# Kernel optimization log

Hardware: AMD Instinct MI355X
Metric: run time of the kernel (lower is better)

The kernel has to match this reference:

```python
import jax, jax.numpy as jnp
import numpy as np

B, S, D, H = 4, 2048, 1024, 16
DK = D // H

def setup_inputs() -> dict:
    key = jax.random.key(0)
    ks = jax.random.split(key, 9)
    sc = 1.0 / np.sqrt(D)
    return {
        "X": jax.random.normal(ks[0], (B, S, D), jnp.float32),
        "Wq": jax.random.normal(ks[1], (D, D), jnp.float32) * sc,
        "bq": jax.random.normal(ks[2], (D,), jnp.float32) * 0.01,
        "Wk": jax.random.normal(ks[3], (D, D), jnp.float32) * sc,
        "bk": jax.random.normal(ks[4], (D,), jnp.float32) * 0.01,
        "Wv": jax.random.normal(ks[5], (D, D), jnp.float32) * sc,
        "bv": jax.random.normal(ks[6], (D,), jnp.float32) * 0.01,
        "Wo": jax.random.normal(ks[7], (D, D), jnp.float32) * sc,
        "bo": jax.random.normal(ks[8], (D,), jnp.float32) * 0.01,
    }

def _split_heads(x):
    b, s, d = x.shape
    return x.reshape(b, s, H, DK).transpose(0, 2, 1, 3)  # [B,H,S,DK]

def reference(X, Wq, bq, Wk, bk, Wv, bv, Wo, bo):
    Q = _split_heads(X @ Wq + bq)
    K = _split_heads(X @ Wk + bk)
    V = _split_heads(X @ Wv + bv)
    scores = jnp.einsum('bhqd,bhkd->bhqk', Q, K) / np.sqrt(DK)  # [B,H,S,S]
    probs = jax.nn.softmax(scores, axis=-1)
    Z = jnp.einsum('bhqk,bhkd->bhqd', probs, V)  # [B,H,S,DK]
    Z = Z.transpose(0, 2, 1, 3).reshape(B, S, D)  # combine heads
    return Z @ Wo + bo
```

## Files before the change

kernel.cpp:

```cpp
#include <hip/hip_runtime.h>

#define Bq 4
#define Sq 2048
#define Dq 1024
#define Hq 16
#define Mq (Bq*Sq)

typedef __attribute__((ext_vector_type(2))) _Float16 f16x2;
typedef __attribute__((ext_vector_type(4))) _Float16 f16x4;
typedef __attribute__((ext_vector_type(8))) _Float16 f16x8;
typedef __attribute__((ext_vector_type(4))) float f32x4;

__device__ __forceinline__ f16x2 cvt_pk_f16(float a, float b) {
  return __builtin_bit_cast(f16x2, __builtin_amdgcn_cvt_pkrtz(a, b));
}

__device__ __forceinline__ float fast_exp2(float x) {
#if __has_builtin(__builtin_amdgcn_exp2f)
  return __builtin_amdgcn_exp2f(x);
#else
  float r;
  asm volatile("v_exp_f32 %0, %1\n\ts_nop 0" : "=v"(r) : "v"(x));
  return r;
#endif
}

__device__ __forceinline__ void gload16(const _Float16* g, _Float16* l) {
  __builtin_amdgcn_global_load_lds(
      (const __attribute__((address_space(1))) unsigned int*)g,
      (__attribute__((address_space(3))) unsigned int*)l, 16, 0, 0);
}

#define VMCNT(n) asm volatile("s_waitcnt vmcnt(" #n ")" ::: "memory")
#define BARRIER() do { __builtin_amdgcn_s_barrier(); __builtin_amdgcn_sched_barrier(0); } while (0)
#define MFMA32(a, b, c) __builtin_amdgcn_mfma_f32_16x16x32_f16(a, b, c, 0, 0, 0)

__global__ void cvt_f32_f16(const float* __restrict__ in, _Float16* __restrict__ out, int n4) {
  int i = blockIdx.x * blockDim.x + threadIdx.x;
  int stride = gridDim.x * blockDim.x;
  for (; i < n4; i += stride) {
    float4 v = ((const float4*)in)[i];
    f16x4 h = { (_Float16)v.x, (_Float16)v.y, (_Float16)v.z, (_Float16)v.w };
    ((f16x4*)out)[i] = h;
  }
}

__global__ __launch_bounds__(256)
void wt_cvt_T(const float* __restrict__ W, _Float16* __restrict__ WT) {
  __shared__ _Float16 Tw[64][68];
  const int t = threadIdx.x;
  const int k0 = blockIdx.x * 64, n0 = blockIdx.y * 64;
  #pragma unroll
  for (int i = 0; i < 4; i++) {
    int row = (t >> 4) + 16 * i;
    float4 v = *(const float4*)(W + (size_t)(k0 + row) * Dq + n0 + (t & 15) * 4);
    f16x4 h = { (_Float16)v.x, (_Float16)v.y, (_Float16)v.z, (_Float16)v.w };
    *(f16x4*)&Tw[row][(t & 15) * 4] = h;
  }
  __syncthreads();
  const int n = t & 63, ks = t >> 6;
  f16x8 v0, v1;
  #pragma unroll
  for (int j = 0; j < 8; j++) { v0[j] = Tw[ks * 16 + j][n]; v1[j] = Tw[ks * 16 + 8 + j][n]; }
  _Float16* dst = WT + (size_t)(n0 + n) * Dq + k0 + ks * 16;
  *(f16x8*)dst = v0;
  *(f16x8*)(dst + 8) = v1;
}

__global__ __launch_bounds__(256, 3)
void qkv_gemm(const _Float16* __restrict__ A, const _Float16* __restrict__ WTall,
              const float* __restrict__ bq, const float* __restrict__ bk,
              const float* __restrict__ bv, _Float16* __restrict__ Qh,
              _Float16* __restrict__ Kh, _Float16* __restrict__ Vth, float qscale) {
  __shared__ alignas(16) char smem[33280];
  _Float16* As = (_Float16*)smem;
  _Float16* Bs = (_Float16*)(smem + 16384);
  const int tid = threadIdx.x, wid = tid >> 6, lane = tid & 63;
  const int wr = wid >> 1, wc = wid & 1;
  const int lq = lane & 15, g = lane >> 4;
  int bid = (int)blockIdx.x;
  bid = (bid & 7) * 192 + (bid >> 3);
  const int bx = bid % 24, by = bid / 24;
  const int row0 = by * 128, col0 = bx * 128;

  const int srow = lane >> 3;
  const int schunk = (lane & 7) ^ srow;
  const _Float16* Ag = A     + (size_t)(row0 + 32 * wid + srow) * Dq + schunk * 8;
  const _Float16* Bg = WTall + (size_t)(col0 + 32 * wid + srow) * Dq + schunk * 8;
  _Float16* AsW = As + (32 * wid) * 64;
  _Float16* BsW = Bs + (32 * wid) * 64;

  f32x4 acc[4][4];
  #pragma unroll
  for (int m = 0; m < 4; m++)
    #pragma unroll
    for (int n = 0; n < 4; n++) acc[m][n] = (f32x4){0.f, 0.f, 0.f, 0.f};

  for (int k0 = 0; k0 < Dq; k0 += 64) {
    __syncthreads();
    #pragma unroll
    for (int i = 0; i < 4; i++) {
      gload16(Ag + k0 + (size_t)(8 * i) * Dq, AsW + (8 * i) * 64);
      gload16(Bg + k0 + (size_t)(8 * i) * Dq, BsW + (8 * i) * 64);
    }
    __syncthreads();
    #pragma unroll
    for (int s = 0; s < 2; s++) {
      f16x8 a[4], b[4];
      #pragma unroll
      for (int m = 0; m < 4; m++) {
        int row = wr * 64 + m * 16 + lq;
        a[m] = *(const f16x8*)&As[row * 64 + (((4 * s + g) ^ (lq & 7)) * 8)];
      }
      #pragma unroll
      for (int n = 0; n < 4; n++) {
        int row = wc * 64 + n * 16 + lq;
        b[n] = *(const f16x8*)&Bs[row * 64 + (((4 * s + g) ^ (lq & 7)) * 8)];
      }
      #pragma unroll
      for (int m = 0; m < 4; m++)
        #pragma unroll
        for (int n = 0; n < 4; n++)
          acc[m][n] = MFMA32(a[m], b[n], acc[m][n]);
    }
  }

  const int rid = col0 >> 10, lcol0 = col0 & 1023;
  const float* bp = rid == 0 ? bq : (rid == 1 ? bk : bv);
  const float scl = rid == 0 ? qscale : 1.0f;

  if (rid < 2) {
    _Float16* Cc = rid == 0 ? Qh : Kh;
    #pragma unroll
    for (int m = 0; m < 4; m++)
      #pragma unroll
      for (int n = 0; n < 4; n++) {
        int col = lcol0 + wc * 64 + n * 16 + lq;
        float bvv = bp[col];
        #pragma unroll
        for (int r = 0; r < 4; r++) {
          int row = row0 + wr * 64 + m * 16 + 4 * g + r;
          Cc[(size_t)row * Dq + col] = (_Float16)((acc[m][n][r] + bvv) * scl);
        }
      }
  } else {
    _Float16* Ts = (_Float16*)smem;
    __syncthreads();
    #pragma unroll
    for (int m = 0; m < 4; m++)
      #pragma unroll
      for (int n = 0; n < 4; n++) {
        int c = wc * 64 + n * 16 + lq;
        float bvv = bp[lcol0 + c];
        #pragma unroll
        for (int r = 0; r < 4; r++) {
          int s = wr * 64 + m * 16 + 4 * g + r;
          Ts[s * 130 + c] = (_Float16)(acc[m][n][r] + bvv);
        }
      }
    __syncthreads();
    const int b = row0 >> 11, stile = (row0 & 2047) >> 7;
    #pragma unroll
    for (int i = 0; i < 8; i++) {
      int idx = i * 256 + tid;
      int hh = idx >> 10, c = idx & 1023;
      int kk = c >> 8, nd = (c >> 6) & 3, gg = (c >> 4) & 3, lqq = c & 15;
      int d = nd * 16 + lqq;
      f16x8 v;
      #pragma unroll
      for (int j = 0; j < 8; j++) {
        int sl = 32 * kk + 16 * (j >> 2) + 4 * gg + (j & 3);
        v[j] = Ts[sl * 130 + hh * 64 + d];
      }
      int hHead = (lcol0 >> 6) + hh;
      size_t off = (((size_t)(b * Hq + hHead) * 16 + stile) * 1024 + c) * 8;
      *(f16x8*)(Vth + off) = v;
    }
  }
}

__global__ __launch_bounds__(256, 3)
void out_gemm(const _Float16* __restrict__ A, const _Float16* __restrict__ WT,
              const float* __restrict__ bias, float* __restrict__ Cf) {
  __shared__ alignas(16) char smem[32768];
  _Float16* As = (_Float16*)smem;
  _Float16* Bs = (_Float16*)(smem + 16384);
  const int tid = threadIdx.x, wid = tid >> 6, lane = tid & 63;
  const int wr = wid >> 1, wc = wid & 1;
  const int lq = lane & 15, g = lane >> 4;
  int bid = (int)blockIdx.x;
  bid = (bid & 7) * 64 + (bid >> 3);
  const int bx = bid & 7, by = bid >> 3;
  const int row0 = by * 128, col0 = bx * 128;

  const int srow = lane >> 3;
  const int schunk = (lane & 7) ^ srow;
  const _Float16* Ag = A  + (size_t)(row0 + 32 * wid + srow) * Dq + schunk * 8;
  const _Float16* Bg = WT + (size_t)(col0 + 32 * wid + srow) * Dq + schunk * 8;
  _Float16* AsW = As + (32 * wid) * 64;
  _Float16* BsW = Bs + (32 * wid) * 64;

  f32x4 acc[4][4];
  #pragma unroll
  for (int m = 0; m < 4; m++)
    #pragma unroll
    for (int n = 0; n < 4; n++) acc[m][n] = (f32x4){0.f, 0.f, 0.f, 0.f};

  for (int k0 = 0; k0 < Dq; k0 += 64) {
    __syncthreads();
    #pragma unroll
    for (int i = 0; i < 4; i++) {
      gload16(Ag + k0 + (size_t)(8 * i) * Dq, AsW + (8 * i) * 64);
      gload16(Bg + k0 + (size_t)(8 * i) * Dq, BsW + (8 * i) * 64);
    }
    __syncthreads();
    #pragma unroll
    for (int s = 0; s < 2; s++) {
      f16x8 a[4], b[4];
      #pragma unroll
      for (int m = 0; m < 4; m++) {
        int row = wr * 64 + m * 16 + lq;
        a[m] = *(const f16x8*)&As[row * 64 + (((4 * s + g) ^ (lq & 7)) * 8)];
      }
      #pragma unroll
      for (int n = 0; n < 4; n++) {
        int row = wc * 64 + n * 16 + lq;
        b[n] = *(const f16x8*)&Bs[row * 64 + (((4 * s + g) ^ (lq & 7)) * 8)];
      }
      #pragma unroll
      for (int m = 0; m < 4; m++)
        #pragma unroll
        for (int n = 0; n < 4; n++)
          acc[m][n] = MFMA32(a[m], b[n], acc[m][n]);
    }
  }

  #pragma unroll
  for (int m = 0; m < 4; m++)
    #pragma unroll
    for (int n = 0; n < 4; n++) {
      int col = col0 + wc * 64 + n * 16 + lq;
      float bvv = bias[col];
      #pragma unroll
      for (int r = 0; r < 4; r++) {
        int row = row0 + wr * 64 + m * 16 + 4 * g + r;
        Cf[(size_t)row * Dq + col] = acc[m][n][r] + bvv;
      }
    }
}

__global__ __launch_bounds__(256, 4)
void attn_kernel(const _Float16* __restrict__ Q, const _Float16* __restrict__ K,
                 const _Float16* __restrict__ Vt, _Float16* __restrict__ Z) {
  __shared__ alignas(16) char smem[32768];
  _Float16* const sm = (_Float16*)smem;
  const int tid = threadIdx.x, wid = tid >> 6, lane = tid & 63;
  const int lq = lane & 15, g = lane >> 4;
  const int id = (int)blockIdx.x;
  const int qb = (id >> 3) & 15;
  const int hb = (id & 7) + 8 * (id >> 7);
  const int h = hb & 15, b = hb >> 4;
  const int q0 = qb * 128;
  const int bh = b * Hq + h;

  const _Float16* Qr0 = Q + (size_t)(b * Sq + q0 + wid * 32 + lq) * Dq + h * 64;
  const _Float16* Qr1 = Qr0 + (size_t)16 * Dq;
  const f16x8 Qf00 = *(const f16x8*)(Qr0 + 8 * g);
  const f16x8 Qf01 = *(const f16x8*)(Qr0 + 32 + 8 * g);
  const f16x8 Qf10 = *(const f16x8*)(Qr1 + 8 * g);
  const f16x8 Qf11 = *(const f16x8*)(Qr1 + 32 + 8 * g);
  VMCNT(0);

  const int krow = tid >> 3;
  const int kch = (tid & 7) ^ (krow & 7);
  const _Float16* Kg = K + (size_t)(b * Sq + krow) * Dq + h * 64 + kch * 8;
  const _Float16* Vg = Vt + (size_t)bh * 16 * 8192;

  const int e7 = lq & 7;
  const int cq0 = (g ^ e7) * 8, cq1 = ((4 + g) ^ e7) * 8;

  f32x4 zacc[2][4];
  #pragma unroll
  for (int gq = 0; gq < 2; gq++)
    #pragma unroll
    for (int nd = 0; nd < 4; nd++) zacc[gq][nd] = (f32x4){0.f, 0.f, 0.f, 0.f};
  f32x4 lsum0 = (f32x4){0.f, 0.f, 0.f, 0.f};
  f32x4 lsum1 = (f32x4){0.f, 0.f, 0.f, 0.f};
  const f32x4 fz = (f32x4){0.f, 0.f, 0.f, 0.f};
  f16x8 ones;
  #pragma unroll
  for (int j = 0; j < 8; j++) ones[j] = (_Float16)1.0f;

  auto stageK = [&](int t, int buf) {
    _Float16* Kd = sm + buf * 4096;
    const _Float16* ks = Kg + (size_t)t * 64 * Dq;
    gload16(ks, Kd + tid * 8);
    gload16(ks + (size_t)32 * Dq, Kd + 2048 + tid * 8);
  };
  auto stageV = [&](int t, int buf) {
    _Float16* Vd = sm + 8192 + buf * 4096;
    const _Float16* vs = Vg + (size_t)(t >> 1) * 8192 + (t & 1) * 4096 + tid * 8;
    gload16(vs, Vd + tid * 8);
    gload16(vs + 2048, Vd + 2048 + tid * 8);
  };

  stageK(0, 0);
  stageV(0, 0);

  for (int t = 0; t < 32; ++t) {
    const int buf = t & 1;
    const _Float16* Kb = sm + buf * 4096;
    const _Float16* Vb = sm + 8192 + buf * 4096;

    if (t) BARRIER();
    if (t < 31) { stageK(t + 1, buf ^ 1); stageV(t + 1, buf ^ 1); VMCNT(4); }
    else        { VMCNT(0); }
    BARRIER();

    f32x4 sacc[2][4];
    __builtin_amdgcn_s_setprio(1);
    #pragma unroll
    for (int rb = 0; rb < 4; ++rb) {
      const _Float16* rbp = Kb + (rb * 16 + lq) * 64;
      f16x8 a0 = *(const f16x8*)(rbp + cq0);
      f16x8 a1 = *(const f16x8*)(rbp + cq1);
      sacc[0][rb] = MFMA32(a0, Qf00, fz);
      sacc[0][rb] = MFMA32(a1, Qf01, sacc[0][rb]);
      sacc[1][rb] = MFMA32(a0, Qf10, fz);
      sacc[1][rb] = MFMA32(a1, Qf11, sacc[1][rb]);
    }
    __builtin_amdgcn_s_setprio(0);

    f16x8 pb[2][2];
    #pragma unroll
    for (int gq = 0; gq < 2; ++gq)
      #pragma unroll
      for (int kkL = 0; kkL < 2; ++kkL) {
        const f32x4 sa = sacc[gq][kkL * 2], sb = sacc[gq][kkL * 2 + 1];
        f16x2 c0 = cvt_pk_f16(fast_exp2(sa[0]), fast_exp2(sa[1]));
        f16x2 c1 = cvt_pk_f16(fast_exp2(sa[2]), fast_exp2(sa[3]));
        f16x2 c2 = cvt_pk_f16(fast_exp2(sb[0]), fast_exp2(sb[1]));
        f16x2 c3 = cvt_pk_f16(fast_exp2(sb[2]), fast_exp2(sb[3]));
        f16x8 p8;
        p8[0] = c0[0]; p8[1] = c0[1]; p8[2] = c1[0]; p8[3] = c1[1];
        p8[4] = c2[0]; p8[5] = c2[1]; p8[6] = c3[0]; p8[7] = c3[1];
        pb[gq][kkL] = p8;
      }

    __builtin_amdgcn_s_setprio(1);
    #pragma unroll
    for (int kkL = 0; kkL < 2; ++kkL) {
      lsum0 = MFMA32(ones, pb[0][kkL], lsum0);
      lsum1 = MFMA32(ones, pb[1][kkL], lsum1);
      #pragma unroll
      for (int nd = 0; nd < 4; ++nd) {
        f16x8 av = *(const f16x8*)(Vb + kkL * 2048 + nd * 512 + lane * 8);
        zacc[0][nd] = MFMA32(av, pb[0][kkL], zacc[0][nd]);
        zacc[1][nd] = MFMA32(av, pb[1][kkL], zacc[1][nd]);
      }
    }
    __builtin_amdgcn_s_setprio(0);
  }

  const float inv0 = 1.0f / lsum0[0];
  const float inv1 = 1.0f / lsum1[0];
  __syncthreads();
  _Float16* Zs = sm;
  #pragma unroll
  for (int gq = 0; gq < 2; gq++) {
    const float inv = gq == 0 ? inv0 : inv1;
    #pragma unroll
    for (int nd = 0; nd < 4; nd++) {
      f16x4 zv;
      #pragma unroll
      for (int r = 0; r < 4; r++) zv[r] = (_Float16)(zacc[gq][nd][r] * inv);
      *(f16x4*)&Zs[(wid * 32 + gq * 16 + lq) * 72 + nd * 16 + 4 * g] = zv;
    }
  }
  __syncthreads();
  const int row = tid >> 1, half = tid & 1;
  const _Float16* zr = &Zs[row * 72 + half * 32];
  f16x8 v0 = *(const f16x8*)zr;
  f16x8 v1 = *(const f16x8*)(zr + 8);
  f16x8 v2 = *(const f16x8*)(zr + 16);
  f16x8 v3 = *(const f16x8*)(zr + 24);
  _Float16* dst = Z + (size_t)(b * Sq + q0 + row) * Dq + h * 64 + half * 32;
  *(f16x8*)dst = v0;
  *(f16x8*)(dst + 8) = v1;
  *(f16x8*)(dst + 16) = v2;
  *(f16x8*)(dst + 24) = v3;
}

extern "C" void kernel_launch(void* const* d_in, const int* in_sizes, int n_in,
                              void* d_out, int out_size, void* d_ws, size_t ws_size,
                              hipStream_t stream) {
  const float* X  = (const float*)d_in[0];
  const float* Wq = (const float*)d_in[1];
  const float* bq = (const float*)d_in[2];
  const float* Wk = (const float*)d_in[3];
  const float* bk = (const float*)d_in[4];
  const float* Wv = (const float*)d_in[5];
  const float* bv = (const float*)d_in[6];
  const float* Wo = (const float*)d_in[7];
  const float* bo = (const float*)d_in[8];

  _Float16* Xh   = (_Float16*)d_ws;
  _Float16* WqT  = Xh   + (size_t)Mq * Dq;
  _Float16* WkT  = WqT  + (size_t)Dq * Dq;
  _Float16* WvT  = WkT  + (size_t)Dq * Dq;
  _Float16* WoT  = WvT  + (size_t)Dq * Dq;
  _Float16* Qh   = WoT  + (size_t)Dq * Dq;
  _Float16* Kh   = Qh   + (size_t)Mq * Dq;
  _Float16* Vth  = Kh   + (size_t)Mq * Dq;
  _Float16* Zh   = Vth  + (size_t)Mq * Dq;

  cvt_f32_f16<<<dim3(2048), dim3(256), 0, stream>>>(X, Xh, (int)((size_t)Mq * Dq / 4));
  dim3 wt(16, 16);
  wt_cvt_T<<<wt, dim3(256), 0, stream>>>(Wq, WqT);
  wt_cvt_T<<<wt, dim3(256), 0, stream>>>(Wk, WkT);
  wt_cvt_T<<<wt, dim3(256), 0, stream>>>(Wv, WvT);
  wt_cvt_T<<<wt, dim3(256), 0, stream>>>(Wo, WoT);

  const float qscale = 0.125f * 1.44269504088896f;
  qkv_gemm<<<dim3(1536), dim3(256), 0, stream>>>(Xh, WqT, bq, bk, bv, Qh, Kh, Vth, qscale);

  attn_kernel<<<dim3(1024), dim3(256), 0, stream>>>(Qh, Kh, Vth, Zh);

  out_gemm<<<dim3(512), dim3(256), 0, stream>>>(Zh, WoT, bo, (float*)d_out);
}
```

Measured before the change: 174.8 us.

## Merge weight conversions into one launch and deepen attention K/V prefetch

The four weight transpose-and-convert launches are merged into a single kernel that selects the weight matrix by block index. The attention loop now prefetches K/V two tiles ahead: it stages tiles 0 and 1 up front and refills a buffer right after its compute, with a barrier in between. The loop is also unrolled by two. The s_nop after the fallback v_exp_f32 asm is dropped. Together these aim to cut launch overhead and hide global load latency, at the cost of an extra barrier per iteration and possible exp hazard timing in the fallback path.

```diff
diff --git a/kernel.cpp b/kernel.cpp
--- a/kernel.cpp
+++ b/kernel.cpp
@@ -20,7 +20,7 @@
   return __builtin_amdgcn_exp2f(x);
 #else
   float r;
-  asm volatile("v_exp_f32 %0, %1\n\ts_nop 0" : "=v"(r) : "v"(x));
+  asm volatile("v_exp_f32 %0, %1" : "=v"(r) : "v"(x));
   return r;
 #endif
 }
@@ -46,10 +46,16 @@
 }
 
 __global__ __launch_bounds__(256)
-void wt_cvt_T(const float* __restrict__ W, _Float16* __restrict__ WT) {
+void wt_cvt_all(const float* __restrict__ W0, const float* __restrict__ W1,
+                const float* __restrict__ W2, const float* __restrict__ W3,
+                _Float16* __restrict__ WTbase) {
   __shared__ _Float16 Tw[64][68];
   const int t = threadIdx.x;
-  const int k0 = blockIdx.x * 64, n0 = blockIdx.y * 64;
+  const int bIdx = (int)blockIdx.x;
+  const int w = bIdx >> 8, r = bIdx & 255;
+  const int k0 = (r & 15) * 64, n0 = (r >> 4) * 64;
+  const float* W = w == 0 ? W0 : (w == 1 ? W1 : (w == 2 ? W2 : W3));
+  _Float16* WT = WTbase + (size_t)w * Dq * Dq;
   #pragma unroll
   for (int i = 0; i < 4; i++) {
     int row = (t >> 4) + 16 * i;
@@ -306,15 +312,16 @@
 
   stageK(0, 0);
   stageV(0, 0);
-
+  stageK(1, 1);
+  stageV(1, 1);
+
+  #pragma unroll 2
   for (int t = 0; t < 32; ++t) {
     const int buf = t & 1;
     const _Float16* Kb = sm + buf * 4096;
     const _Float16* Vb = sm + 8192 + buf * 4096;
 
-    if (t) BARRIER();
-    if (t < 31) { stageK(t + 1, buf ^ 1); stageV(t + 1, buf ^ 1); VMCNT(4); }
-    else        { VMCNT(0); }
+    if (t < 31) { VMCNT(4); } else { VMCNT(0); }
     BARRIER();
 
     f32x4 sacc[2][4];
@@ -360,6 +367,9 @@
       }
     }
     __builtin_amdgcn_s_setprio(0);
+
+    BARRIER();
+    if (t < 30) { stageK(t + 2, buf); stageV(t + 2, buf); }
   }
 
   const float inv0 = 1.0f / lsum0[0];
@@ -406,20 +416,14 @@
 
   _Float16* Xh   = (_Float16*)d_ws;
   _Float16* WqT  = Xh   + (size_t)Mq * Dq;
-  _Float16* WkT  = WqT  + (size_t)Dq * Dq;
-  _Float16* WvT  = WkT  + (size_t)Dq * Dq;
-  _Float16* WoT  = WvT  + (size_t)Dq * Dq;
+  _Float16* WoT  = WqT  + (size_t)3 * Dq * Dq;
   _Float16* Qh   = WoT  + (size_t)Dq * Dq;
   _Float16* Kh   = Qh   + (size_t)Mq * Dq;
   _Float16* Vth  = Kh   + (size_t)Mq * Dq;
   _Float16* Zh   = Vth  + (size_t)Mq * Dq;
 
   cvt_f32_f16<<<dim3(2048), dim3(256), 0, stream>>>(X, Xh, (int)((size_t)Mq * Dq / 4));
-  dim3 wt(16, 16);
-  wt_cvt_T<<<wt, dim3(256), 0, stream>>>(Wq, WqT);
-  wt_cvt_T<<<wt, dim3(256), 0, stream>>>(Wk, WkT);
-  wt_cvt_T<<<wt, dim3(256), 0, stream>>>(Wv, WvT);
-  wt_cvt_T<<<wt, dim3(256), 0, stream>>>(Wo, WoT);
+  wt_cvt_all<<<dim3(1024), dim3(256), 0, stream>>>(Wq, Wk, Wv, Wo, WqT);
 
   const float qscale = 0.125f * 1.44269504088896f;
   qkv_gemm<<<dim3(1536), dim3(256), 0, stream>>>(Xh, WqT, bq, bk, bv, Qh, Kh, Vth, qscale);
```

Measured after the change: 168.4 us. -3.7%, faster.
